# Kernel tuning notes

Measured on AMD Instinct MI355X. Metric: run time of the kernel, lower is better.

Reference implementation:

```python
import jax, jax.numpy as jnp
import numpy as np

LR = 0.3
AT = 0.0
DSBETA = 1e-4
EPS_DS = 1e-2

def setup_inputs() -> dict:
    key = jax.random.key(0)
    k1, k2, k3 = jax.random.split(key, 3)
    B, D, N = 65536, 256, 1024
    x = jax.random.normal(k1, (B, D), jnp.float32)
    weights = jax.random.normal(k2, (N, D), jnp.float32)
    moving_avg = jax.random.uniform(k3, (N, D), jnp.float32) * 0.1
    relevance = jnp.ones((N, D), jnp.float32)
    node_control = jnp.ones((N,), jnp.float32)
    return {"x": x, "weights": weights, "moving_avg": moving_avg,
            "relevance": relevance, "node_control": node_control}


def reference(x, weights, moving_avg, relevance, node_control):
    # SOM.forward, high-activation branch, expressed with fixed shapes:
    # per-node outputs are padded to the full [n_max, D] table and masked by
    # `has` (node received >=1 high-activation sample), which is the jit-safe
    # equivalent of torch.unique + fancy-index scatter on unique BMU ids.
    B, D = x.shape
    N = weights.shape[0]
    rel_sum = relevance.sum(axis=1)                                   # [N]
    # pairwise squared distance [B, N]
    d = ((x * x).sum(axis=1)[:, None] + (weights * weights).sum(axis=1)[None, :]
         - 2.0 * (x @ weights.T))
    dw = d * (rel_sum / D)[None, :]                                   # weighted_distance
    dw = jnp.where(jnp.isnan(dw), 0.0, dw)
    act = (rel_sum / (rel_sum + dw + 1e-7)) * node_control[None, :]   # activation * node_control
    idx = jnp.argmax(act, axis=1)                                     # BMU per sample
    act_max = jnp.max(act, axis=1)
    high = (act_max >= AT).astype(x.dtype)                            # [B]
    # unique_node_diff_vectorized: per-BMU mean of assigned high samples
    counts = jax.ops.segment_sum(high, idx, num_segments=N)           # [N]
    sums = jax.ops.segment_sum(x * high[:, None], idx, num_segments=N)  # [N, D]
    has = counts > 0
    avg_samples = sums / jnp.maximum(counts, 1.0)[:, None]            # [N, D]
    # update_node on nodes with has
    distance = jnp.abs(avg_samples - weights)
    a = LR * DSBETA
    ma_new = a * distance + (1.0 - a) * moving_avg
    ma_upd = jnp.where(has[:, None], ma_new, moving_avg)
    # NOTE: in torch, index has shape [1, n_unique] so moving_avg[index] is
    # [1, n_unique, D] and max/min/mean over dim=1 reduce ACROSS unique nodes,
    # per feature. Replicate that exactly with masked reductions over nodes.
    neg_inf = jnp.array(-jnp.inf, x.dtype)
    pos_inf = jnp.array(jnp.inf, x.dtype)
    mx = jnp.max(jnp.where(has[:, None], ma_new, neg_inf), axis=0)    # [D]
    mn = jnp.min(jnp.where(has[:, None], ma_new, pos_inf), axis=0)    # [D]
    n_has = jnp.maximum(has.sum().astype(x.dtype), 1.0)
    avg = jnp.sum(jnp.where(has[:, None], ma_new, 0.0), axis=0) / n_has  # [D]
    rel_new = 1.0 / (1.0 + jnp.exp((ma_new - avg[None, :]) / (EPS_DS * (mx - mn)[None, :])))
    rel_new = jnp.where(jnp.isnan(rel_new), 1.0, rel_new)
    rel_upd = jnp.where(has[:, None], rel_new, relevance)
    delta = jnp.where(has[:, None], LR * (avg_samples - weights), 0.0)
    w_upd = weights + delta
    loss = delta.sum() / B
    return avg_samples, w_upd, ma_upd, rel_upd, loss
```

## Files before the change

### kernel.cpp

```cpp
#include <hip/hip_runtime.h>
#include <math.h>

constexpr int DD = 256;
constexpr int NN = 1024;
constexpr float C_LR = 0.3f;
constexpr float C_DSBETA = 1e-4f;
constexpr float C_EPS_DS = 1e-2f;

using short8  = __attribute__((ext_vector_type(8))) short;
using f32x16  = __attribute__((ext_vector_type(16))) float;

__device__ __forceinline__ unsigned short f2bf(float f) {
    unsigned u = __float_as_uint(f);
    u += 0x7FFF + ((u >> 16) & 1);
    return (unsigned short)(u >> 16);
}
__device__ __forceinline__ float bf2f(unsigned short h) {
    return __uint_as_float(((unsigned)h) << 16);
}

__global__ __launch_bounds__(256) void k_init(
    const float* __restrict__ w, const float* __restrict__ rel,
    unsigned short* __restrict__ wh_g, unsigned short* __restrict__ wl_g,
    float* __restrict__ wn2, float* __restrict__ rsum,
    int* __restrict__ counts, float* __restrict__ sums,
    unsigned* __restrict__ mx_bits, unsigned* __restrict__ mn_bits,
    float* __restrict__ avgsum, int* __restrict__ n_has, float* __restrict__ loss_acc)
{
    int n = blockIdx.x, t = threadIdx.x;
    size_t o = (size_t)n * DD + t;
    float wv = w[o];
    unsigned short hi = f2bf(wv);
    float lo = wv - bf2f(hi);
    wh_g[o] = hi;
    wl_g[o] = f2bf(lo);
    sums[o] = 0.f;
    __shared__ float sA[256], sB[256];
    sA[t] = wv * wv; sB[t] = rel[o];
    __syncthreads();
    #pragma unroll
    for (int s = 128; s >= 1; s >>= 1) {
        if (t < s) { sA[t] += sA[t + s]; sB[t] += sB[t + s]; }
        __syncthreads();
    }
    if (t == 0) { wn2[n] = sA[0]; rsum[n] = sB[0]; counts[n] = 0; }
    if (n == 0) {
        mx_bits[t] = 0u;
        mn_bits[t] = 0x7F800000u;
        avgsum[t] = 0.f;
        if (t == 0) { *n_has = 0; *loss_acc = 0.f; }
    }
}

__global__ __launch_bounds__(256, 2) void k_main(
    const float* __restrict__ x, const float* __restrict__ wf,
    const unsigned short* __restrict__ wh_g, const unsigned short* __restrict__ wl_g,
    const float* __restrict__ ncontrol, const float* __restrict__ wn2,
    const float* __restrict__ rsum,
    int* __restrict__ counts, float* __restrict__ sums)
{
    __shared__ __align__(16) unsigned char smem[65536];
    __shared__ float xn2_l[64];
    __shared__ unsigned long long key_l[64][2][2];
    __shared__ int cand_l[64][2];
    __shared__ double resc[64][2];
    __shared__ int bmu_l[64];

    const int t = threadIdx.x;
    const int lane = t & 63;
    const int w = t >> 6;
    const int wm = w >> 1, wn = w & 1;
    const int m0 = wm * 32;
    const int l31 = lane & 31, half = lane >> 5;
    const int bb = blockIdx.x * 64;

    const int grow = bb + m0 + l31;
    short8 xh[16], xl[16];
    float xn2p = 0.f;
    const float* xr = x + (size_t)grow * DD + half * 8;
    #pragma unroll
    for (int s = 0; s < 16; ++s) {
        float4 a = *(const float4*)(xr + s * 16);
        float4 b = *(const float4*)(xr + s * 16 + 4);
        float f[8] = {a.x, a.y, a.z, a.w, b.x, b.y, b.z, b.w};
        #pragma unroll
        for (int j = 0; j < 8; ++j) {
            xn2p += f[j] * f[j];
            unsigned short hi = f2bf(f[j]);
            float lo = f[j] - bf2f(hi);
            xh[s][j] = (short)hi;
            xl[s][j] = (short)f2bf(lo);
        }
    }
    xn2p += __shfl_xor(xn2p, 32);
    if (wn == 0 && half == 0) xn2_l[m0 + l31] = xn2p;
    __syncthreads();

    float xn2r[16];
    #pragma unroll
    for (int r = 0; r < 16; ++r)
        xn2r[r] = xn2_l[m0 + (r & 3) + 8 * (r >> 2) + 4 * half];

    unsigned long long bestk[16], bestk2[16];
    #pragma unroll
    for (int r = 0; r < 16; ++r) { bestk[r] = 0ull; bestk2[r] = 0ull; }

    const int swz = l31 << 4;
    const int nlrow = wn * 32 + l31;
    const unsigned char* bhbase = smem + nlrow * 512;
    const unsigned char* blbase = smem + 32768 + nlrow * 512;

    for (int nt = 0; nt < 16; ++nt) {
        int ng = nt * 64 + nlrow;
        float wn2v = wn2[ng], rsv = rsum[ng], ncv = ncontrol[ng];

        #pragma unroll
        for (int p = 0; p < 16; ++p) {
            int g = p * 256 + t;
            int r = g >> 6, c = g & 63;
            size_t go = (size_t)(nt * 64 + r) * DD + c * 4;
            int loff = r * 512 + ((c * 8) ^ ((r & 31) << 4));
            *(ushort4*)(smem + loff)         = *(const ushort4*)(wh_g + go);
            *(ushort4*)(smem + 32768 + loff) = *(const ushort4*)(wl_g + go);
        }
        __syncthreads();

        f32x16 acc;
        #pragma unroll
        for (int r = 0; r < 16; ++r) acc[r] = 0.f;

        #pragma unroll
        for (int s = 0; s < 16; ++s) {
            int koff = (s * 32 + half * 16) ^ swz;
            short8 bh = *(const short8*)(bhbase + koff);
            short8 bl = *(const short8*)(blbase + koff);
            acc = __builtin_amdgcn_mfma_f32_32x32x16_bf16(xh[s], bh, acc, 0, 0, 0);
            acc = __builtin_amdgcn_mfma_f32_32x32x16_bf16(xl[s], bh, acc, 0, 0, 0);
            acc = __builtin_amdgcn_mfma_f32_32x32x16_bf16(xh[s], bl, acc, 0, 0, 0);
        }

        float rvd  = rsv * (1.f / 256.f);
        float den0 = rsv + 1e-7f;
        float num  = rsv * ncv;
        unsigned inv_n = (unsigned)(NN - 1 - ng);
        #pragma unroll
        for (int r = 0; r < 16; ++r) {
            float d   = xn2r[r] + wn2v - 2.f * acc[r];
            float den = den0 + d * rvd;
            float act = num * __builtin_amdgcn_rcpf(den);
            unsigned long long key =
                ((unsigned long long)(__float_as_uint(act) | 0x80000000u) << 32) | inv_n;
            if (key > bestk[r]) { bestk2[r] = bestk[r]; bestk[r] = key; }
            else if (key > bestk2[r]) bestk2[r] = key;
        }
        __syncthreads();
    }

    #pragma unroll
    for (int mask = 1; mask <= 16; mask <<= 1) {
        #pragma unroll
        for (int r = 0; r < 16; ++r) {
            unsigned long long ob = __shfl_xor(bestk[r], mask);
            unsigned long long os = __shfl_xor(bestk2[r], mask);
            if (ob > bestk[r]) {
                bestk2[r] = (bestk[r] > os) ? bestk[r] : os;
                bestk[r]  = ob;
            } else {
                if (ob > bestk2[r]) bestk2[r] = ob;
            }
        }
    }
    if (l31 == 0) {
        #pragma unroll
        for (int r = 0; r < 16; ++r) {
            int mrow = (r & 3) + 8 * (r >> 2) + 4 * half;
            key_l[m0 + mrow][wn][0] = bestk[r];
            key_l[m0 + mrow][wn][1] = bestk2[r];
        }
    }
    __syncthreads();

    if (t < 64) {
        unsigned long long b0k = key_l[t][0][0], s0k = key_l[t][0][1];
        unsigned long long b1k = key_l[t][1][0], s1k = key_l[t][1][1];
        unsigned long long B, S;
        if (b0k > b1k) { B = b0k; S = (s0k > b1k) ? s0k : b1k; }
        else           { B = b1k; S = (s1k > b0k) ? s1k : b0k; }
        cand_l[t][0] = (NN - 1) - (int)(B & 0xFFFFFFFFull);
        cand_l[t][1] = (NN - 1) - (int)(S & 0xFFFFFFFFull);
    }
    __syncthreads();

    if (t < 128) {
        int s = t >> 1, c = t & 1;
        int node = cand_l[s][c];
        const float* xr2 = x + (size_t)(bb + s) * DD;
        const float* wr2 = wf + (size_t)node * DD;
        double a = 0.0;
        #pragma unroll 4
        for (int k = 0; k < DD; k += 4) {
            float4 xv = *(const float4*)(xr2 + k);
            float4 wv = *(const float4*)(wr2 + k);
            double d0 = (double)xv.x - (double)wv.x;
            double d1 = (double)xv.y - (double)wv.y;
            double d2 = (double)xv.z - (double)wv.z;
            double d3 = (double)xv.w - (double)wv.w;
            a += d0 * d0 + d1 * d1 + d2 * d2 + d3 * d3;
        }
        double rs = (double)rsum[node];
        double dw = a * rs * (1.0 / 256.0);
        double act = rs / (rs + dw + 1e-7) * (double)ncontrol[node];
        resc[s][c] = act;
    }
    __syncthreads();

    if (t < 64) {
        int c0 = cand_l[t][0], c1 = cand_l[t][1];
        double a0 = resc[t][0], a1 = resc[t][1];
        int bmu = c0;
        if (a1 > a0 || (a1 == a0 && c1 < c0)) bmu = c1;
        bmu_l[t] = bmu;
        atomicAdd(&counts[bmu], 1);
    }
    __syncthreads();

    #pragma unroll 4
    for (int s2 = 0; s2 < 64; ++s2) {
        atomicAdd(&sums[(size_t)bmu_l[s2] * DD + t], x[(size_t)(bb + s2) * DD + t]);
    }
}

__global__ __launch_bounds__(256) void k_node(
    const float* __restrict__ w, const float* __restrict__ ma,
    const int* __restrict__ counts, const float* __restrict__ sums,
    float* __restrict__ out_avg, float* __restrict__ out_w, float* __restrict__ out_ma,
    unsigned* __restrict__ mx_bits, unsigned* __restrict__ mn_bits,
    float* __restrict__ avgsum, int* __restrict__ n_has, float* __restrict__ loss_acc)
{
    int n = blockIdx.x, t = threadIdx.x;
    int cnt = counts[n];
    size_t o = (size_t)n * DD + t;
    bool has = cnt > 0;
    float avg = has ? sums[o] / (float)cnt : 0.f;
    float wv = w[o], mav = ma[o];
    out_avg[o] = avg;
    float dist = fabsf(avg - wv);
    const float a = C_LR * C_DSBETA;
    float man = a * dist + (1.f - a) * mav;
    out_ma[o] = has ? man : mav;
    float delta = has ? C_LR * (avg - wv) : 0.f;
    out_w[o] = wv + delta;
    if (has) {
        atomicMax(&mx_bits[t], __float_as_uint(man));
        atomicMin(&mn_bits[t], __float_as_uint(man));
        atomicAdd(&avgsum[t], man);
        if (t == 0) atomicAdd(n_has, 1);
    }
    __shared__ float rs[256];
    rs[t] = delta;
    __syncthreads();
    #pragma unroll
    for (int s2 = 128; s2 >= 1; s2 >>= 1) {
        if (t < s2) rs[t] += rs[t + s2];
        __syncthreads();
    }
    if (t == 0) atomicAdd(loss_acc, rs[0]);
}

__global__ __launch_bounds__(256) void k_rel(
    const float* __restrict__ rel_in, const float* __restrict__ out_ma,
    const int* __restrict__ counts,
    const unsigned* __restrict__ mx_bits, const unsigned* __restrict__ mn_bits,
    const float* __restrict__ avgsum, const int* __restrict__ n_has,
    const float* __restrict__ loss_acc,
    float* __restrict__ out_rel, float* __restrict__ out_loss, float invB)
{
    int n = blockIdx.x, t = threadIdx.x;
    size_t o = (size_t)n * DD + t;
    bool has = counts[n] > 0;
    float r;
    if (has) {
        float nh  = fmaxf((float)(*n_has), 1.f);
        float avg = avgsum[t] / nh;
        float mx  = __uint_as_float(mx_bits[t]);
        float mn  = __uint_as_float(mn_bits[t]);
        float man = out_ma[o];
        float targ = (man - avg) / (C_EPS_DS * (mx - mn));
        float e = expf(targ);
        float rr = 1.f / (1.f + e);
        if (!(rr == rr)) rr = 1.f;
        r = rr;
    } else {
        r = rel_in[o];
    }
    out_rel[o] = r;
    if (n == 0 && t == 0) *out_loss = (*loss_acc) * invB;
}

extern "C" void kernel_launch(void* const* d_in, const int* in_sizes, int n_in,
                              void* d_out, int out_size, void* d_ws, size_t ws_size,
                              hipStream_t stream)
{
    const float* x   = (const float*)d_in[0];
    const float* w   = (const float*)d_in[1];
    const float* ma  = (const float*)d_in[2];
    const float* rel = (const float*)d_in[3];
    const float* nc  = (const float*)d_in[4];

    const int B = in_sizes[0] / DD;
    const int ND = NN * DD;

    float* out      = (float*)d_out;
    float* out_avg  = out;
    float* out_w    = out + ND;
    float* out_ma   = out + 2 * ND;
    float* out_rel  = out + 3 * ND;
    float* out_loss = out + 4 * ND;

    char* ws = (char*)d_ws;
    size_t off = 0;
    float* sums   = (float*)(ws + off); off += (size_t)ND * 4;
    unsigned short* wh_g = (unsigned short*)(ws + off); off += (size_t)ND * 2;
    unsigned short* wl_g = (unsigned short*)(ws + off); off += (size_t)ND * 2;
    int* counts   = (int*)(ws + off); off += NN * 4;
    float* wn2    = (float*)(ws + off); off += NN * 4;
    float* rsum   = (float*)(ws + off); off += NN * 4;
    unsigned* mxb = (unsigned*)(ws + off); off += DD * 4;
    unsigned* mnb = (unsigned*)(ws + off); off += DD * 4;
    float* avgsum = (float*)(ws + off); off += DD * 4;
    int* n_has    = (int*)(ws + off); off += 256;
    float* loss_a = (float*)(ws + off); off += 256;

    k_init<<<NN, 256, 0, stream>>>(w, rel, wh_g, wl_g, wn2, rsum, counts, sums,
                                   mxb, mnb, avgsum, n_has, loss_a);
    k_main<<<B / 64, 256, 0, stream>>>(x, w, wh_g, wl_g, nc, wn2, rsum, counts, sums);
    k_node<<<NN, 256, 0, stream>>>(w, ma, counts, sums,
                                   out_avg, out_w, out_ma, mxb, mnb, avgsum, n_has, loss_a);
    k_rel<<<NN, 256, 0, stream>>>(rel, out_ma, counts, mxb, mnb, avgsum, n_has, loss_a,
                                  out_rel, out_loss, 1.0f / (float)B);
}
```

Baseline: 749.3 us.

## Replace float atomic scatter of samples with counting-sort gather per node

Measured after the change: 934.2 us. +24.7%, slower.

```diff
diff --git a/kernel.cpp b/kernel.cpp
--- a/kernel.cpp
+++ b/kernel.cpp
@@ -22,8 +22,7 @@
 __global__ __launch_bounds__(256) void k_init(
     const float* __restrict__ w, const float* __restrict__ rel,
     unsigned short* __restrict__ wh_g, unsigned short* __restrict__ wl_g,
-    float* __restrict__ wn2, float* __restrict__ rsum,
-    int* __restrict__ counts, float* __restrict__ sums,
+    float* __restrict__ wn2, float* __restrict__ rsum, int* __restrict__ counts,
     unsigned* __restrict__ mx_bits, unsigned* __restrict__ mn_bits,
     float* __restrict__ avgsum, int* __restrict__ n_has, float* __restrict__ loss_acc)
 {
@@ -34,7 +33,6 @@
     float lo = wv - bf2f(hi);
     wh_g[o] = hi;
     wl_g[o] = f2bf(lo);
-    sums[o] = 0.f;
     __shared__ float sA[256], sB[256];
     sA[t] = wv * wv; sB[t] = rel[o];
     __syncthreads();
@@ -57,14 +55,13 @@
     const unsigned short* __restrict__ wh_g, const unsigned short* __restrict__ wl_g,
     const float* __restrict__ ncontrol, const float* __restrict__ wn2,
     const float* __restrict__ rsum,
-    int* __restrict__ counts, float* __restrict__ sums)
+    int* __restrict__ counts, int* __restrict__ bmu_g)
 {
     __shared__ __align__(16) unsigned char smem[65536];
     __shared__ float xn2_l[64];
     __shared__ unsigned long long key_l[64][2][2];
     __shared__ int cand_l[64][2];
     __shared__ double resc[64][2];
-    __shared__ int bmu_l[64];
 
     const int t = threadIdx.x;
     const int lane = t & 63;
@@ -219,29 +216,68 @@
         double a0 = resc[t][0], a1 = resc[t][1];
         int bmu = c0;
         if (a1 > a0 || (a1 == a0 && c1 < c0)) bmu = c1;
-        bmu_l[t] = bmu;
+        bmu_g[bb + t] = bmu;
         atomicAdd(&counts[bmu], 1);
     }
-    __syncthreads();
-
-    #pragma unroll 4
-    for (int s2 = 0; s2 < 64; ++s2) {
-        atomicAdd(&sums[(size_t)bmu_l[s2] * DD + t], x[(size_t)(bb + s2) * DD + t]);
-    }
+}
+
+__global__ __launch_bounds__(256) void k_scan(
+    const int* __restrict__ counts, int* __restrict__ offsets, int* __restrict__ cursor)
+{
+    __shared__ int s[256];
+    int t = threadIdx.x;
+    int base = t * 4;
+    int c0 = counts[base], c1 = counts[base + 1], c2 = counts[base + 2], c3 = counts[base + 3];
+    int loc = c0 + c1 + c2 + c3;
+    s[t] = loc;
+    __syncthreads();
+    for (int off = 1; off < 256; off <<= 1) {
+        int v = (t >= off) ? s[t - off] : 0;
+        __syncthreads();
+        s[t] += v;
+        __syncthreads();
+    }
+    int excl = s[t] - loc;
+    offsets[base] = excl;           cursor[base] = excl;
+    offsets[base + 1] = excl + c0;  cursor[base + 1] = excl + c0;
+    offsets[base + 2] = excl + c0 + c1;      cursor[base + 2] = excl + c0 + c1;
+    offsets[base + 3] = excl + c0 + c1 + c2; cursor[base + 3] = excl + c0 + c1 + c2;
+}
+
+__global__ __launch_bounds__(256) void k_scatter(
+    const int* __restrict__ bmu_g, int* __restrict__ cursor, int* __restrict__ order)
+{
+    int b = blockIdx.x * 256 + threadIdx.x;
+    int n = bmu_g[b];
+    int p = atomicAdd(&cursor[n], 1);
+    order[p] = b;
 }
 
 __global__ __launch_bounds__(256) void k_node(
-    const float* __restrict__ w, const float* __restrict__ ma,
-    const int* __restrict__ counts, const float* __restrict__ sums,
+    const float* __restrict__ x, const float* __restrict__ w, const float* __restrict__ ma,
+    const int* __restrict__ counts, const int* __restrict__ offsets, const int* __restrict__ order,
     float* __restrict__ out_avg, float* __restrict__ out_w, float* __restrict__ out_ma,
     unsigned* __restrict__ mx_bits, unsigned* __restrict__ mn_bits,
     float* __restrict__ avgsum, int* __restrict__ n_has, float* __restrict__ loss_acc)
 {
     int n = blockIdx.x, t = threadIdx.x;
-    int cnt = counts[n];
+    int cnt = counts[n], base = offsets[n];
+    float s = 0.f;
+    int j = 0;
+    for (; j + 4 <= cnt; j += 4) {
+        int b0 = order[base + j], b1 = order[base + j + 1];
+        int b2 = order[base + j + 2], b3 = order[base + j + 3];
+        float v0 = x[(size_t)b0 * DD + t];
+        float v1 = x[(size_t)b1 * DD + t];
+        float v2 = x[(size_t)b2 * DD + t];
+        float v3 = x[(size_t)b3 * DD + t];
+        s += (v0 + v1) + (v2 + v3);
+    }
+    for (; j < cnt; ++j) s += x[(size_t)order[base + j] * DD + t];
+
+    bool has = cnt > 0;
+    float avg = has ? s / (float)cnt : 0.f;
     size_t o = (size_t)n * DD + t;
-    bool has = cnt > 0;
-    float avg = has ? sums[o] / (float)cnt : 0.f;
     float wv = w[o], mav = ma[o];
     out_avg[o] = avg;
     float dist = fabsf(avg - wv);
@@ -319,10 +355,13 @@
 
     char* ws = (char*)d_ws;
     size_t off = 0;
-    float* sums   = (float*)(ws + off); off += (size_t)ND * 4;
     unsigned short* wh_g = (unsigned short*)(ws + off); off += (size_t)ND * 2;
     unsigned short* wl_g = (unsigned short*)(ws + off); off += (size_t)ND * 2;
+    int* bmu_g    = (int*)(ws + off); off += (size_t)B * 4;
+    int* order    = (int*)(ws + off); off += (size_t)B * 4;
     int* counts   = (int*)(ws + off); off += NN * 4;
+    int* offsets  = (int*)(ws + off); off += NN * 4;
+    int* cursor   = (int*)(ws + off); off += NN * 4;
     float* wn2    = (float*)(ws + off); off += NN * 4;
     float* rsum   = (float*)(ws + off); off += NN * 4;
     unsigned* mxb = (unsigned*)(ws + off); off += DD * 4;
@@ -331,10 +370,12 @@
     int* n_has    = (int*)(ws + off); off += 256;
     float* loss_a = (float*)(ws + off); off += 256;
 
-    k_init<<<NN, 256, 0, stream>>>(w, rel, wh_g, wl_g, wn2, rsum, counts, sums,
+    k_init<<<NN, 256, 0, stream>>>(w, rel, wh_g, wl_g, wn2, rsum, counts,
                                    mxb, mnb, avgsum, n_has, loss_a);
-    k_main<<<B / 64, 256, 0, stream>>>(x, w, wh_g, wl_g, nc, wn2, rsum, counts, sums);
-    k_node<<<NN, 256, 0, stream>>>(w, ma, counts, sums,
+    k_main<<<B / 64, 256, 0, stream>>>(x, w, wh_g, wl_g, nc, wn2, rsum, counts, bmu_g);
+    k_scan<<<1, 256, 0, stream>>>(counts, offsets, cursor);
+    k_scatter<<<B / 256, 256, 0, stream>>>(bmu_g, cursor, order);
+    k_node<<<NN, 256, 0, stream>>>(x, w, ma, counts, offsets, order,
                                    out_avg, out_w, out_ma, mxb, mnb, avgsum, n_has, loss_a);
     k_rel<<<NN, 256, 0, stream>>>(rel, out_ma, counts, mxb, mnb, avgsum, n_has, loss_a,
                                   out_rel, out_loss, 1.0f / (float)B);
```

## Split weights to bf16 hi/lo inside main kernel and reuse x from registers for scatter

Applied to the files above, without the earlier changes.

Measured after the change: 840.3 us. +12.1%, slower.

```diff
diff --git a/kernel.cpp b/kernel.cpp
--- a/kernel.cpp
+++ b/kernel.cpp
@@ -21,19 +21,14 @@
 
 __global__ __launch_bounds__(256) void k_init(
     const float* __restrict__ w, const float* __restrict__ rel,
-    unsigned short* __restrict__ wh_g, unsigned short* __restrict__ wl_g,
-    float* __restrict__ wn2, float* __restrict__ rsum,
-    int* __restrict__ counts, float* __restrict__ sums,
+    float* __restrict__ wn2, float* __restrict__ rsum, int* __restrict__ counts,
+    float* __restrict__ sums,
     unsigned* __restrict__ mx_bits, unsigned* __restrict__ mn_bits,
     float* __restrict__ avgsum, int* __restrict__ n_has, float* __restrict__ loss_acc)
 {
     int n = blockIdx.x, t = threadIdx.x;
     size_t o = (size_t)n * DD + t;
     float wv = w[o];
-    unsigned short hi = f2bf(wv);
-    float lo = wv - bf2f(hi);
-    wh_g[o] = hi;
-    wl_g[o] = f2bf(lo);
     sums[o] = 0.f;
     __shared__ float sA[256], sB[256];
     sA[t] = wv * wv; sB[t] = rel[o];
@@ -54,12 +49,11 @@
 
 __global__ __launch_bounds__(256, 2) void k_main(
     const float* __restrict__ x, const float* __restrict__ wf,
-    const unsigned short* __restrict__ wh_g, const unsigned short* __restrict__ wl_g,
     const float* __restrict__ ncontrol, const float* __restrict__ wn2,
     const float* __restrict__ rsum,
     int* __restrict__ counts, float* __restrict__ sums)
 {
-    __shared__ __align__(16) unsigned char smem[65536];
+    __shared__ __align__(16) unsigned char smem[66560];
     __shared__ float xn2_l[64];
     __shared__ unsigned long long key_l[64][2][2];
     __shared__ int cand_l[64][2];
@@ -109,6 +103,7 @@
     const int nlrow = wn * 32 + l31;
     const unsigned char* bhbase = smem + nlrow * 512;
     const unsigned char* blbase = smem + 32768 + nlrow * 512;
+    const float4* wf4 = (const float4*)wf;
 
     for (int nt = 0; nt < 16; ++nt) {
         int ng = nt * 64 + nlrow;
@@ -118,10 +113,17 @@
         for (int p = 0; p < 16; ++p) {
             int g = p * 256 + t;
             int r = g >> 6, c = g & 63;
-            size_t go = (size_t)(nt * 64 + r) * DD + c * 4;
+            float4 v = wf4[(size_t)(nt * 64 + r) * 64 + c];
+            float fs[4] = {v.x, v.y, v.z, v.w};
+            ushort4 hv, lv;
+            unsigned short hj;
+            hj = f2bf(fs[0]); hv.x = hj; lv.x = f2bf(fs[0] - bf2f(hj));
+            hj = f2bf(fs[1]); hv.y = hj; lv.y = f2bf(fs[1] - bf2f(hj));
+            hj = f2bf(fs[2]); hv.z = hj; lv.z = f2bf(fs[2] - bf2f(hj));
+            hj = f2bf(fs[3]); hv.w = hj; lv.w = f2bf(fs[3] - bf2f(hj));
             int loff = r * 512 + ((c * 8) ^ ((r & 31) << 4));
-            *(ushort4*)(smem + loff)         = *(const ushort4*)(wh_g + go);
-            *(ushort4*)(smem + 32768 + loff) = *(const ushort4*)(wl_g + go);
+            *(ushort4*)(smem + loff)         = hv;
+            *(ushort4*)(smem + 32768 + loff) = lv;
         }
         __syncthreads();
 
@@ -222,11 +224,30 @@
         bmu_l[t] = bmu;
         atomicAdd(&counts[bmu], 1);
     }
-    __syncthreads();
-
+
+    float* xf = (float*)smem;
+    __syncthreads();
+    if (wn == 0) {
+        float* dst = xf + (m0 + l31) * 260 + half * 8;
+        #pragma unroll
+        for (int s = 0; s < 16; ++s) {
+            float4 v0, v1;
+            v0.x = bf2f((unsigned short)xh[s][0]) + bf2f((unsigned short)xl[s][0]);
+            v0.y = bf2f((unsigned short)xh[s][1]) + bf2f((unsigned short)xl[s][1]);
+            v0.z = bf2f((unsigned short)xh[s][2]) + bf2f((unsigned short)xl[s][2]);
+            v0.w = bf2f((unsigned short)xh[s][3]) + bf2f((unsigned short)xl[s][3]);
+            v1.x = bf2f((unsigned short)xh[s][4]) + bf2f((unsigned short)xl[s][4]);
+            v1.y = bf2f((unsigned short)xh[s][5]) + bf2f((unsigned short)xl[s][5]);
+            v1.z = bf2f((unsigned short)xh[s][6]) + bf2f((unsigned short)xl[s][6]);
+            v1.w = bf2f((unsigned short)xh[s][7]) + bf2f((unsigned short)xl[s][7]);
+            *(float4*)(dst + s * 16)     = v0;
+            *(float4*)(dst + s * 16 + 4) = v1;
+        }
+    }
+    __syncthreads();
     #pragma unroll 4
     for (int s2 = 0; s2 < 64; ++s2) {
-        atomicAdd(&sums[(size_t)bmu_l[s2] * DD + t], x[(size_t)(bb + s2) * DD + t]);
+        atomicAdd(&sums[(size_t)bmu_l[s2] * DD + t], xf[s2 * 260 + t]);
     }
 }
 
@@ -320,8 +341,6 @@
     char* ws = (char*)d_ws;
     size_t off = 0;
     float* sums   = (float*)(ws + off); off += (size_t)ND * 4;
-    unsigned short* wh_g = (unsigned short*)(ws + off); off += (size_t)ND * 2;
-    unsigned short* wl_g = (unsigned short*)(ws + off); off += (size_t)ND * 2;
     int* counts   = (int*)(ws + off); off += NN * 4;
     float* wn2    = (float*)(ws + off); off += NN * 4;
     float* rsum   = (float*)(ws + off); off += NN * 4;
@@ -331,9 +350,9 @@
     int* n_has    = (int*)(ws + off); off += 256;
     float* loss_a = (float*)(ws + off); off += 256;
 
-    k_init<<<NN, 256, 0, stream>>>(w, rel, wh_g, wl_g, wn2, rsum, counts, sums,
+    k_init<<<NN, 256, 0, stream>>>(w, rel, wn2, rsum, counts, sums,
                                    mxb, mnb, avgsum, n_has, loss_a);
-    k_main<<<B / 64, 256, 0, stream>>>(x, w, wh_g, wl_g, nc, wn2, rsum, counts, sums);
+    k_main<<<B / 64, 256, 0, stream>>>(x, w, nc, wn2, rsum, counts, sums);
     k_node<<<NN, 256, 0, stream>>>(w, ma, counts, sums,
                                    out_avg, out_w, out_ma, mxb, mnb, avgsum, n_has, loss_a);
     k_rel<<<NN, 256, 0, stream>>>(rel, out_ma, counts, mxb, mnb, avgsum, n_has, loss_a,
```
